# Kernel tuning notes

Measured on AMD Instinct MI355X. Metric: run time of the kernel, lower is better.

## Reference

```python
import jax, jax.numpy as jnp
import numpy as np

B, T, C, H = 2, 2048, 1024, 16
N = C // H
MISS_ROWS = 128


def _rwkv7_scan(q, w_log, k, v, a, b):
    # all [B,T,H,N] float32 (bf16-rounded). RWKV7 delta-rule recurrence:
    #   S_t = S_{t-1} * diag(exp(w_t)) + (S_{t-1} a_t) b_t^T + v_t k_t^T
    #   o_t = S_t q_t   (state S has shape [B,H,Nv,Nk]; decay along k-dim)
    Bq, Tq, Hq, Nq = q.shape

    def step(S, inp):
        q_t, w_t, k_t, v_t, a_t, b_t = inp
        ew = jnp.exp(w_t)  # decay in (0,1) since w_log = -exp(...) < 0
        sa = jnp.einsum('bhvi,bhi->bhv', S, a_t)
        S = S * ew[:, :, None, :] + sa[..., None] * b_t[:, :, None, :] + v_t[..., None] * k_t[:, :, None, :]
        o = jnp.einsum('bhvj,bhj->bhv', S, q_t)
        return S, o

    xs = tuple(jnp.moveaxis(u, 1, 0) for u in (q, w_log, k, v, a, b))
    S0 = jnp.zeros((Bq, Hq, Nq, Nq), jnp.float32)
    _, o = jax.lax.scan(step, S0, xs)
    return jnp.moveaxis(o, 0, 1)  # [B,T,H,N]


def setup_inputs() -> dict:
    key = jax.random.key(0)
    ks = jax.random.split(key, 16)
    f32 = jnp.float32
    return {
        'residual': jax.random.normal(ks[0], (B, T, C), f32),
        'x': jax.random.normal(ks[1], (B, T, C), f32),
        'x0': jax.random.normal(ks[2], (B, T, C), f32),
        'dx0': jax.random.normal(ks[3], (B, T, C), f32),
        'Wq': jax.random.normal(ks[4], (C, C), f32) * 0.02,
        'Wk': jax.random.normal(ks[5], (C, C), f32) * 0.02,
        'Wv': jax.random.normal(ks[6], (C, C), f32) * 0.02,
        'Wproj': jax.random.normal(ks[7], (C, C), f32) * 0.02,
        'x_q': jax.random.uniform(ks[8], (1, 1, C), f32),
        'x_k': jax.random.uniform(ks[9], (1, 1, C), f32),
        'x_v': jax.random.uniform(ks[10], (1, 1, C), f32),
        'v0': 0.7 + 0.1 * jax.random.normal(ks[11], (1, 1, C), f32),
        'w0': -3.0 + 0.5 * jax.random.normal(ks[12], (1, 1, C), f32),
        'a0': 0.1 * jax.random.normal(ks[13], (1, 1, C), f32),
        'miss': jax.random.normal(ks[14], (MISS_ROWS, 4 * C), f32) * 0.02,
        'r_k': 0.1 * jax.random.normal(ks[15], (H, N), f32),
    }


def reference(residual, x, x0, dx0, Wq, Wk, Wv, Wproj, x_q, x_k, x_v, v0, w0, a0, miss, r_k):
    Bx, Tx, Cx = x.shape
    Hh, Nn = r_k.shape
    # token shift: dx_prev = x_{t-1} - x_t (zero-padded at t=0)
    dx_prev = jnp.concatenate([jnp.zeros_like(x[:, :1]), x[:, :-1]], axis=1) - x
    q = (x + dx_prev * x_q) @ Wq.T
    k = (x + dx_prev * x_k) @ Wk.T
    v = (x + dx_prev * x_v) @ Wv.T
    deltas = x[:, :, :miss.shape[0]] @ miss  # [B,T,4C]
    w_delta, v_delta, a_delta, g = jnp.split(deltas, 4, axis=-1)
    log_neglog_w = -jax.nn.softplus(-(w0 + w_delta)) - 0.5
    log_w = -jnp.exp(log_neglog_w)  # log decay, always < 0
    v_first = (x0 + dx0 * x_v) @ Wv.T
    v = v + (v_first - v) * jax.nn.sigmoid(v0 + v_delta)
    g = 1.0 + g
    a = jax.nn.sigmoid(a0 + a_delta)
    kh = k.reshape(Bx, Tx, Hh, Nn)
    kk = kh / jnp.maximum(jnp.linalg.norm(kh, axis=-1, keepdims=True), 1e-12)
    kk = kk.reshape(Bx, Tx, Cx)
    k = k * a
    z = -kk
    b = kk * a
    bf = lambda u: u.astype(jnp.bfloat16).astype(jnp.float32).reshape(Bx, Tx, Hh, Nn)
    qh, wh, kh2, vh, zh, bh = (bf(u) for u in (q, log_w, k, v, z, b))
    y = _rwkv7_scan(qh, wh, kh2, vh, zh, bh) * (float(Nn) ** -0.5)  # [B,T,H,N]
    xnorm = jnp.linalg.norm(x.reshape(Bx, Tx, Hh, Nn), axis=-1, keepdims=True)
    vnorm = jnp.linalg.norm(vh, axis=-1, keepdims=True)
    u = (1.0 - xnorm / (vnorm + 1e-12)) * jax.nn.sigmoid(r_k)
    y = (y + vh * u).reshape(Bx, Tx, Cx)
    y = y * g
    return residual + y @ Wproj.T
```

## Files before the change

kernel.cpp:

```cpp
#include <hip/hip_runtime.h>
#include <stdint.h>
#include <stddef.h>

#define B_ 2
#define T_ 2048
#define C_ 1024
#define H_ 16
#define N_ 64
#define M_ (B_*T_)
#define L_ 128
#define NC_ (T_/L_)

typedef unsigned short ushort_t;
typedef __attribute__((ext_vector_type(8))) __bf16 bf16x8;
typedef __attribute__((ext_vector_type(4))) float  f32x4;

__device__ __forceinline__ ushort_t f2bf(float x){
  uint32_t u = __float_as_uint(x);
  u += 0x7fffu + ((u >> 16) & 1u);
  return (ushort_t)(u >> 16);
}
__device__ __forceinline__ float bf2f(uint32_t hu){
  return __uint_as_float(hu << 16);
}
__device__ __forceinline__ float quad_sum(float v){
  float a = __int_as_float(__builtin_amdgcn_mov_dpp(__float_as_int(v), 0xB1, 0xF, 0xF, true));
  v += a;
  float b = __int_as_float(__builtin_amdgcn_mov_dpp(__float_as_int(v), 0x4E, 0xF, 0xF, true));
  return v + b;
}

__device__ __forceinline__ ushort4 mixq4(float4 a, float4 p, float4 c){
  ushort4 o;
  o.x = f2bf(fmaf(p.x - a.x, c.x, a.x));
  o.y = f2bf(fmaf(p.y - a.y, c.y, a.y));
  o.z = f2bf(fmaf(p.z - a.z, c.z, a.z));
  o.w = f2bf(fmaf(p.w - a.w, c.w, a.w));
  return o;
}
__global__ __launch_bounds__(256) void prep_all(
    const float* __restrict__ x, const float* __restrict__ x0,
    const float* __restrict__ dx0,
    const float* __restrict__ xq, const float* __restrict__ xk,
    const float* __restrict__ xv,
    const float* __restrict__ Wq, const float* __restrict__ Wk,
    const float* __restrict__ Wv, const float* __restrict__ Wp,
    const float* __restrict__ miss,
    ushort_t* __restrict__ Aq, ushort_t* __restrict__ Ak,
    ushort_t* __restrict__ Av, ushort_t* __restrict__ Axf,
    ushort_t* __restrict__ Xb,
    ushort_t* __restrict__ Wb, ushort_t* __restrict__ Wpb,
    ushort_t* __restrict__ missT)
{
  __shared__ ushort_t tile[128][66];
  const int blk = blockIdx.x;
  const int tid = threadIdx.x;
  if (blk < 4096){
    const int idx = blk*256 + tid;
    const int col4 = idx & 255;
    const int i = idx >> 8;
    const int t = i & (T_-1);
    float4 a = ((const float4*)x)[idx];
    float4 p = {0.f,0.f,0.f,0.f};
    if (t > 0) p = ((const float4*)x)[idx - 256];
    float4 cq = ((const float4*)xq)[col4];
    float4 ck = ((const float4*)xk)[col4];
    float4 cv = ((const float4*)xv)[col4];
    ((ushort4*)Aq)[idx] = mixq4(a, p, cq);
    ((ushort4*)Ak)[idx] = mixq4(a, p, ck);
    ((ushort4*)Av)[idx] = mixq4(a, p, cv);
    float4 z = ((const float4*)x0)[idx];
    float4 d = ((const float4*)dx0)[idx];
    ushort4 of;
    of.x = f2bf(fmaf(d.x, cv.x, z.x));
    of.y = f2bf(fmaf(d.y, cv.y, z.y));
    of.z = f2bf(fmaf(d.z, cv.z, z.z));
    of.w = f2bf(fmaf(d.w, cv.w, z.w));
    ((ushort4*)Axf)[idx] = of;
    ushort4 ob = {f2bf(a.x), f2bf(a.y), f2bf(a.z), f2bf(a.w)};
    ((ushort4*)Xb)[idx] = ob;
  } else if (blk < 4096 + 5*1024){
    const int y = (blk - 4096) >> 10;
    const float* src = (y==0)?Wq:(y==1)?Wk:(y<4)?Wv:Wp;
    ushort_t* dst = (y<4) ? Wb + (size_t)y*C_*C_ : Wpb;
    const int idx = ((blk - 4096) & 1023)*256 + tid;
    float4 v = ((const float4*)src)[idx];
    ushort4 o = {f2bf(v.x), f2bf(v.y), f2bf(v.z), f2bf(v.w)};
    ((ushort4*)dst)[idx] = o;
  } else {
    const int j0 = (blk - 4096 - 5*1024)*64;
#pragma unroll
    for (int rep=0; rep<8; rep++){
      int k = rep*16 + (tid>>4);
      int jj = (tid&15)*4;
      float4 v = *(const float4*)&miss[(size_t)k*4096 + j0 + jj];
      tile[k][jj+0]=f2bf(v.x); tile[k][jj+1]=f2bf(v.y);
      tile[k][jj+2]=f2bf(v.z); tile[k][jj+3]=f2bf(v.w);
    }
    __syncthreads();
#pragma unroll
    for (int rep=0; rep<8; rep++){
      int j = tid>>2;
      int kk = (tid&3)*32 + rep*4;
      ushort4 o = {tile[kk+0][j], tile[kk+1][j], tile[kk+2][j], tile[kk+3][j]};
      *(ushort4*)&missT[(size_t)(j0+j)*128 + kk] = o;
    }
  }
}

__global__ __launch_bounds__(256, 2) void mfma_gemm(
    const ushort_t* __restrict__ Ab, int lda, int64_t Asz,
    const ushort_t* __restrict__ Bbp, int ldb, int64_t Bsz,
    void* __restrict__ Cb, int ldc, int64_t Csz, int c_bf16,
    const float* __restrict__ resid, int K)
{
  const ushort_t* A  = Ab  + (size_t)blockIdx.z * Asz;
  const ushort_t* Bm = Bbp + (size_t)blockIdx.z * Bsz;
  const int i0 = blockIdx.y * 128;
  const int j0 = blockIdx.x * 128;
  const int tid = threadIdx.x;
  const int lane = tid & 63;
  const int w = tid >> 6;
  const int wm = w & 1, wn = w >> 1;

  __shared__ ushort_t As[128*32];
  __shared__ ushort_t Bs[128*32];

  f32x4 acc[4][4];
#pragma unroll
  for (int i=0;i<4;i++)
#pragma unroll
    for (int j=0;j<4;j++) acc[i][j] = (f32x4){0.f,0.f,0.f,0.f};

  const int lr = lane >> 2;
  const int ls = lane & 3;
  const ushort_t* ga = A  + (size_t)(i0 + w*32 + lr)*lda + ls*8;
  const ushort_t* gb = Bm + (size_t)(j0 + w*32 + lr)*ldb + ls*8;
  const int lm = lane & 15, lq = lane >> 4;

  for (int k0 = 0; k0 < K; k0 += 32){
    __syncthreads();
#pragma unroll
    for (int p=0;p<2;p++){
      __builtin_amdgcn_global_load_lds(
        (const __attribute__((address_space(1))) void*)(ga + (size_t)p*16*lda + k0),
        (__attribute__((address_space(3))) void*)&As[(w*32 + p*16)*32], 16, 0, 0);
      __builtin_amdgcn_global_load_lds(
        (const __attribute__((address_space(1))) void*)(gb + (size_t)p*16*ldb + k0),
        (__attribute__((address_space(3))) void*)&Bs[(w*32 + p*16)*32], 16, 0, 0);
    }
    __syncthreads();
    bf16x8 af[4], bfr[4];
#pragma unroll
    for (int i=0;i<4;i++)
      af[i] = *(const bf16x8*)&As[(wm*64 + i*16 + lm)*32 + lq*8];
#pragma unroll
    for (int j=0;j<4;j++)
      bfr[j] = *(const bf16x8*)&Bs[(wn*64 + j*16 + lm)*32 + lq*8];
#pragma unroll
    for (int i=0;i<4;i++)
#pragma unroll
      for (int j=0;j<4;j++)
        acc[i][j] = __builtin_amdgcn_mfma_f32_16x16x32_bf16(af[i], bfr[j], acc[i][j], 0, 0, 0);
  }

  if (!c_bf16){
    float* C = (float*)Cb + (size_t)blockIdx.z * Csz;
#pragma unroll
    for (int i=0;i<4;i++)
#pragma unroll
      for (int j=0;j<4;j++)
#pragma unroll
        for (int r=0;r<4;r++){
          const int row = i0 + wm*64 + i*16 + lq*4 + r;
          const int col = j0 + wn*64 + j*16 + lm;
          float v = acc[i][j][r];
          if (resid) v += resid[(size_t)row*ldc + col];
          C[(size_t)row*ldc + col] = v;
        }
  } else {
    ushort_t* C = (ushort_t*)Cb + (size_t)blockIdx.z * Csz;
#pragma unroll
    for (int i=0;i<4;i++)
#pragma unroll
      for (int j=0;j<4;j++)
#pragma unroll
        for (int r=0;r<4;r++){
          const int row = i0 + wm*64 + i*16 + lq*4 + r;
          const int col = j0 + wn*64 + j*16 + lm;
          C[(size_t)row*ldc + col] = f2bf(acc[i][j][r]);
        }
  }
}

__global__ __launch_bounds__(256, 2) void qkvm_gemm(
    const ushort_t* __restrict__ Ab4, const ushort_t* __restrict__ Wb,
    const ushort_t* __restrict__ Xb,  const ushort_t* __restrict__ missT,
    float* __restrict__ qkvf, ushort_t* __restrict__ delb)
{
  const int bid = blockIdx.x;
  const bool isQKV = bid < 1024;
  const ushort_t* A; const ushort_t* Bm;
  int i0, j0, ldb, K, z = 0;
  if (isQKV){
    z = bid >> 8;
    const int g = bid & 255;
    j0 = (g & 7) * 128;
    i0 = (g >> 3) * 128;
    A  = Ab4 + (size_t)z*M_*C_;
    Bm = Wb  + (size_t)z*C_*C_;
    ldb = C_; K = C_;
  } else {
    const int g = bid - 1024;
    j0 = (g & 31) * 128;
    i0 = (g >> 5) * 128;
    A = Xb; Bm = missT;
    ldb = 128; K = 128;
  }
  const int lda = C_;
  const int tid = threadIdx.x;
  const int lane = tid & 63;
  const int w = tid >> 6;
  const int wm = w & 1, wn = w >> 1;

  __shared__ ushort_t As[128*32];
  __shared__ ushort_t Bs[128*32];

  f32x4 acc[4][4];
#pragma unroll
  for (int i=0;i<4;i++)
#pragma unroll
    for (int j=0;j<4;j++) acc[i][j] = (f32x4){0.f,0.f,0.f,0.f};

  const int lr = lane >> 2;
  const int ls = lane & 3;
  const ushort_t* ga = A  + (size_t)(i0 + w*32 + lr)*lda + ls*8;
  const ushort_t* gb = Bm + (size_t)(j0 + w*32 + lr)*ldb + ls*8;
  const int lm = lane & 15, lq = lane >> 4;

  for (int k0 = 0; k0 < K; k0 += 32){
    __syncthreads();
#pragma unroll
    for (int p=0;p<2;p++){
      __builtin_amdgcn_global_load_lds(
        (const __attribute__((address_space(1))) void*)(ga + (size_t)p*16*lda + k0),
        (__attribute__((address_space(3))) void*)&As[(w*32 + p*16)*32], 16, 0, 0);
      __builtin_amdgcn_global_load_lds(
        (const __attribute__((address_space(1))) void*)(gb + (size_t)p*16*ldb + k0),
        (__attribute__((address_space(3))) void*)&Bs[(w*32 + p*16)*32], 16, 0, 0);
    }
    __syncthreads();
    bf16x8 af[4], bfr[4];
#pragma unroll
    for (int i=0;i<4;i++)
      af[i] = *(const bf16x8*)&As[(wm*64 + i*16 + lm)*32 + lq*8];
#pragma unroll
    for (int j=0;j<4;j++)
      bfr[j] = *(const bf16x8*)&Bs[(wn*64 + j*16 + lm)*32 + lq*8];
#pragma unroll
    for (int i=0;i<4;i++)
#pragma unroll
      for (int j=0;j<4;j++)
        acc[i][j] = __builtin_amdgcn_mfma_f32_16x16x32_bf16(af[i], bfr[j], acc[i][j], 0, 0, 0);
  }

  if (isQKV){
    float* C = qkvf + (size_t)z*M_*C_;
#pragma unroll
    for (int i=0;i<4;i++)
#pragma unroll
      for (int j=0;j<4;j++)
#pragma unroll
        for (int r=0;r<4;r++){
          const int row = i0 + wm*64 + i*16 + lq*4 + r;
          const int col = j0 + wn*64 + j*16 + lm;
          C[(size_t)row*C_ + col] = acc[i][j][r];
        }
  } else {
#pragma unroll
    for (int i=0;i<4;i++)
#pragma unroll
      for (int j=0;j<4;j++)
#pragma unroll
        for (int r=0;r<4;r++){
          const int row = i0 + wm*64 + i*16 + lq*4 + r;
          const int col = j0 + wn*64 + j*16 + lm;
          delb[(size_t)row*(4*C_) + col] = f2bf(acc[i][j][r]);
        }
  }
}


__global__ __launch_bounds__(512, 4) void chunk_mdp_kernel(
    const float* __restrict__ qm, const float* __restrict__ km,
    const float* __restrict__ vm, const float* __restrict__ vfm,
    const float* __restrict__ x, const ushort_t* __restrict__ delb,
    const float* __restrict__ w0, const float* __restrict__ v0,
    const float* __restrict__ a0,
    float* __restrict__ phi, float* __restrict__ cc, float* __restrict__ md,
    ushort_t* __restrict__ vb, float* __restrict__ ratio)
{
  const int tid  = threadIdx.x;
  const int role = tid >> 8;
  const int row  = (tid >> 2) & 63;
  const int qr   = tid & 3;

  __shared__ float ewS[8][N_], zS[8][N_], bS[8][N_], kS[8][N_], qS[8][N_], vS[8][N_];

  const int g  = blockIdx.x;
  const int cx = g & (NC_-1), bh = g >> 4;
  const int b = bh >> 4, h = bh & 15;
  const int t0 = b*T_ + cx*L_;

  const int ls = tid >> 6;
  const int ld = tid & 63;
  const int cdim = h*64 + ld;
  const float w0c = w0[cdim], v0c = v0[cdim], a0c = a0[cdim];

  float pq, pk, pv, pvf, px;
  ushort_t dwd, dvd, dad;
  float Few, Fz, Fb, Fk, Fq, Fv, Fratio;
  ushort_t Fvr;

#define LOAD_RAW(T_IDX) { \
    size_t ic = (size_t)(t0 + (T_IDX))*C_ + cdim; \
    pq = qm[ic]; pk = km[ic]; pv = vm[ic]; pvf = vfm[ic]; px = x[ic]; \
    size_t d0 = (size_t)(t0 + (T_IDX))*4*C_ + cdim; \
    dwd = delb[d0]; dvd = delb[d0+C_]; dad = delb[d0+2*C_]; }

#define FUSE_RAW() { \
    float wd = bf2f(dwd), vd = bf2f(dvd), ad = bf2f(dad); \
    float z1 = -(w0c + wd); \
    float sp = fmaxf(z1, 0.f) + log1pf(expf(-fabsf(z1))); \
    float logw = -expf(-sp - 0.5f); \
    float sv = 1.f/(1.f+expf(-(v0c + vd))); \
    float vvm = pv + (pvf - pv)*sv; \
    float av = 1.f/(1.f+expf(-(a0c + ad))); \
    Fvr = f2bf(vvm); \
    float vrf = bf2f(Fvr); \
    float ksq = pk*pk, xsq = px*px, vsq = vrf*vrf; \
    _Pragma("unroll") \
    for (int off=32; off>0; off>>=1){ \
      ksq += __shfl_xor(ksq, off, 64); \
      xsq += __shfl_xor(xsq, off, 64); \
      vsq += __shfl_xor(vsq, off, 64); \
    } \
    float kn = sqrtf(ksq); \
    float kkn = pk / fmaxf(kn, 1e-12f); \
    Few = __expf(bf2f(f2bf(logw))); \
    Fz = bf2f(f2bf(-kkn)); \
    Fb = bf2f(f2bf(kkn*av)); \
    Fk = bf2f(f2bf(pk*av)); \
    Fq = bf2f(f2bf(pq)); \
    Fv = vrf; \
    Fratio = 1.f - sqrtf(xsq)/(sqrtf(vsq)+1e-12f); }

  LOAD_RAW(ls);
  FUSE_RAW();

  float R[16];
  if (role == 0){
#pragma unroll
    for (int i=0;i<16;i++) R[i] = (qr*16+i == row) ? 1.f : 0.f;
  } else {
#pragma unroll
    for (int i=0;i<16;i++) R[i] = 0.f;
  }

  for (int tg = 0; tg < L_; tg += 8){
    __syncthreads();
    ewS[ls][ld] = Few;
    zS[ls][ld]  = Fz;
    bS[ls][ld]  = Fb;
    kS[ls][ld]  = Fk;
    qS[ls][ld]  = Fq;
    vS[ls][ld]  = Fv;
    {
      const int tok = t0 + tg + ls;
      vb[(size_t)tok*C_ + cdim] = Fvr;
      if (ld == 0)
        ratio[(size_t)tok*H_ + h] = Fratio;
    }
    if (tg + 8 < L_) LOAD_RAW(tg+8+ls);
    __syncthreads();
#pragma unroll 1
    for (int ss=0; ss<8; ss++){
      const float* zr = &zS[ss][qr*16];
      float s_ = 0.f;
#pragma unroll
      for (int i4=0;i4<4;i4++){
        float4 z4 = *(const float4*)&zr[i4*4];
        s_ = fmaf(R[i4*4+0], z4.x, s_);
        s_ = fmaf(R[i4*4+1], z4.y, s_);
        s_ = fmaf(R[i4*4+2], z4.z, s_);
        s_ = fmaf(R[i4*4+3], z4.w, s_);
      }
      s_ = quad_sum(s_);
      const float* er = &ewS[ss][qr*16];
      const float* br = &bS[ss][qr*16];
      const float* qrp = &qS[ss][qr*16];
      float o = 0.f;
      if (role == 0){
#pragma unroll
        for (int i4=0;i4<4;i4++){
          float4 e4 = *(const float4*)&er[i4*4];
          float4 b4 = *(const float4*)&br[i4*4];
          float4 q4 = *(const float4*)&qrp[i4*4];
          float t;
          t = fmaf(R[i4*4+0], e4.x, s_*b4.x); R[i4*4+0]=t; o = fmaf(t, q4.x, o);
          t = fmaf(R[i4*4+1], e4.y, s_*b4.y); R[i4*4+1]=t; o = fmaf(t, q4.y, o);
          t = fmaf(R[i4*4+2], e4.z, s_*b4.z); R[i4*4+2]=t; o = fmaf(t, q4.z, o);
          t = fmaf(R[i4*4+3], e4.w, s_*b4.w); R[i4*4+3]=t; o = fmaf(t, q4.w, o);
        }
      } else {
        const float* kr = &kS[ss][qr*16];
        const float vr = vS[ss][row];
#pragma unroll
        for (int i4=0;i4<4;i4++){
          float4 e4 = *(const float4*)&er[i4*4];
          float4 b4 = *(const float4*)&br[i4*4];
          float4 q4 = *(const float4*)&qrp[i4*4];
          float4 k4 = *(const float4*)&kr[i4*4];
          float t;
          t = fmaf(R[i4*4+0], e4.x, fmaf(s_, b4.x, vr*k4.x)); R[i4*4+0]=t; o = fmaf(t, q4.x, o);
          t = fmaf(R[i4*4+1], e4.y, fmaf(s_, b4.y, vr*k4.y)); R[i4*4+1]=t; o = fmaf(t, q4.y, o);
          t = fmaf(R[i4*4+2], e4.z, fmaf(s_, b4.z, vr*k4.z)); R[i4*4+2]=t; o = fmaf(t, q4.z, o);
          t = fmaf(R[i4*4+3], e4.w, fmaf(s_, b4.w, vr*k4.w)); R[i4*4+3]=t; o = fmaf(t, q4.w, o);
        }
      }
      o = quad_sum(o);
      if (qr == 0)
        md[((size_t)g*L_ + tg+ss)*128 + role*64 + row] = o;
    }
    if (tg + 8 < L_) FUSE_RAW();
  }
  float* dst = (role == 0) ? phi : cc;
  const size_t base = (size_t)g*4096 + (size_t)row*64 + qr*16;
#pragma unroll
  for (int i4=0;i4<4;i4++)
    *(float4*)&dst[base + i4*4] = (float4){R[i4*4+0],R[i4*4+1],R[i4*4+2],R[i4*4+3]};
#undef LOAD_RAW
#undef FUSE_RAW
}

__global__ __launch_bounds__(256) void chunk_state_kernel(
    const float* __restrict__ phi, const float* __restrict__ cc,
    float* __restrict__ sstart)
{
  const int mq = blockIdx.x;
  const int bh = blockIdx.y;
  const int tid = threadIdx.x;
  const int rb = tid >> 4;
  const int cq = tid & 15;
  const int row = mq*16 + rb;
  __shared__ float Sld[16][65];
  __shared__ float Fld[64][68];
  float acc[4] = {0.f, 0.f, 0.f, 0.f};
  *(float4*)&Sld[rb][cq*4] = (float4){0.f,0.f,0.f,0.f};
  const float* pc = phi + (size_t)bh*NC_*4096;
  const float* cb = cc  + (size_t)bh*NC_*4096;
  float4 pf[4], pcc;
#pragma unroll
  for (int p=0;p<4;p++) pf[p] = *(const float4*)&pc[(size_t)p*1024 + tid*4];
  pcc = *(const float4*)&cb[(size_t)row*64 + cq*4];

  for (int c=0;c<NC_;c++){
    __syncthreads();
#pragma unroll
    for (int p=0;p<4;p++){
      int f = p*1024 + tid*4;
      *(float4*)&Fld[f>>6][f&63] = pf[p];
    }
    float na[4] = {pcc.x, pcc.y, pcc.z, pcc.w};
    *(float4*)&sstart[(size_t)(bh*NC_+c)*4096 + (size_t)row*64 + cq*4] =
        (float4){acc[0],acc[1],acc[2],acc[3]};
    if (c+1 < NC_){
#pragma unroll
      for (int p=0;p<4;p++) pf[p] = *(const float4*)&pc[(size_t)(c+1)*4096 + p*1024 + tid*4];
      pcc = *(const float4*)&cb[(size_t)(c+1)*4096 + (size_t)row*64 + cq*4];
    }
    __syncthreads();
#pragma unroll 1
    for (int k0=0;k0<64;k0+=4){
      const float4 sr = *(const float4*)&Sld[rb][k0];
      const float4 f0 = *(const float4*)&Fld[k0+0][cq*4];
      const float4 f1 = *(const float4*)&Fld[k0+1][cq*4];
      const float4 f2 = *(const float4*)&Fld[k0+2][cq*4];
      const float4 f3 = *(const float4*)&Fld[k0+3][cq*4];
      na[0] = fmaf(sr.x, f0.x, na[0]); na[0] = fmaf(sr.y, f1.x, na[0]);
      na[0] = fmaf(sr.z, f2.x, na[0]); na[0] = fmaf(sr.w, f3.x, na[0]);
      na[1] = fmaf(sr.x, f0.y, na[1]); na[1] = fmaf(sr.y, f1.y, na[1]);
      na[1] = fmaf(sr.z, f2.y, na[1]); na[1] = fmaf(sr.w, f3.y, na[1]);
      na[2] = fmaf(sr.x, f0.z, na[2]); na[2] = fmaf(sr.y, f1.z, na[2]);
      na[2] = fmaf(sr.z, f2.z, na[2]); na[2] = fmaf(sr.w, f3.z, na[2]);
      na[3] = fmaf(sr.x, f0.w, na[3]); na[3] = fmaf(sr.y, f1.w, na[3]);
      na[3] = fmaf(sr.z, f2.w, na[3]); na[3] = fmaf(sr.w, f3.w, na[3]);
    }
    __syncthreads();
    *(float4*)&Sld[rb][cq*4] = (float4){na[0],na[1],na[2],na[3]};
#pragma unroll
    for (int i=0;i<4;i++) acc[i] = na[i];
  }
}

__global__ __launch_bounds__(256) void chunk_emit_kernel(
    const ushort_t* __restrict__ vb, const ushort_t* __restrict__ delb,
    const float* __restrict__ ratio, const float* __restrict__ rk,
    const float* __restrict__ sstart, const float* __restrict__ md,
    ushort_t* __restrict__ y)
{
  const int blk = blockIdx.x;
  const int c  = blk & (NC_-1);
  const int bh = blk >> 4;
  const int b = bh >> 4, h = bh & 15;
  const int tid = threadIdx.x;
  const int v = tid & 63;
  const int tg = tid >> 6;

  float4 sr[16];
  const float4* sp = (const float4*)(sstart + (size_t)blk*4096 + (size_t)v*64);
#pragma unroll
  for (int f=0;f<16;f++) sr[f] = sp[f];
  const float sigrk = 1.f/(1.f+__expf(-rk[h*64+v]));

#pragma unroll 1
  for (int ss=0; ss<32; ss++){
    const int t = tg*32 + ss;
    const int token = b*T_ + c*L_ + t;
    const float* mrow = md + ((size_t)blk*L_ + t)*128;
    float o0=0.f,o1=0.f,o2=0.f,o3=0.f;
#pragma unroll
    for (int f=0;f<16;f+=4){
      float4 m0 = ((const float4*)mrow)[f+0];
      float4 m1 = ((const float4*)mrow)[f+1];
      float4 m2 = ((const float4*)mrow)[f+2];
      float4 m3 = ((const float4*)mrow)[f+3];
      o0 = fmaf(sr[f+0].x,m0.x, fmaf(sr[f+0].y,m0.y, fmaf(sr[f+0].z,m0.z, fmaf(sr[f+0].w,m0.w, o0))));
      o1 = fmaf(sr[f+1].x,m1.x, fmaf(sr[f+1].y,m1.y, fmaf(sr[f+1].z,m1.z, fmaf(sr[f+1].w,m1.w, o1))));
      o2 = fmaf(sr[f+2].x,m2.x, fmaf(sr[f+2].y,m2.y, fmaf(sr[f+2].z,m2.z, fmaf(sr[f+2].w,m2.w, o2))));
      o3 = fmaf(sr[f+3].x,m3.x, fmaf(sr[f+3].y,m3.y, fmaf(sr[f+3].z,m3.z, fmaf(sr[f+3].w,m3.w, o3))));
    }
    float o = ((o0+o1)+(o2+o3)) + mrow[64 + v];
    const float vt = bf2f(vb[(size_t)token*C_ + h*64 + v]);
    const float uv = ratio[(size_t)token*H_ + h];
    const float gv = 1.f + bf2f(delb[(size_t)token*4*C_ + 3*C_ + h*64 + v]);
    y[(size_t)token*C_ + h*64 + v] = f2bf((o*0.125f + vt*uv*sigrk)*gv);
  }
}

extern "C" void kernel_launch(void* const* d_in, const int* in_sizes, int n_in,
                              void* d_out, int out_size, void* d_ws, size_t ws_size,
                              hipStream_t stream)
{
  const float* residual = (const float*)d_in[0];
  const float* x    = (const float*)d_in[1];
  const float* x0   = (const float*)d_in[2];
  const float* dx0  = (const float*)d_in[3];
  const float* Wq   = (const float*)d_in[4];
  const float* Wk   = (const float*)d_in[5];
  const float* Wv   = (const float*)d_in[6];
  const float* Wpr  = (const float*)d_in[7];
  const float* x_q  = (const float*)d_in[8];
  const float* x_k  = (const float*)d_in[9];
  const float* x_v  = (const float*)d_in[10];
  const float* v0   = (const float*)d_in[11];
  const float* w0   = (const float*)d_in[12];
  const float* a0   = (const float*)d_in[13];
  const float* miss = (const float*)d_in[14];
  const float* rk   = (const float*)d_in[15];
  float* out = (float*)d_out;

  char* ws = (char*)d_ws;
  const size_t MB = (size_t)1 << 20;
  float*    q_m    = (float*)(ws + 0*MB);
  float*    k_m    = (float*)(ws + 16*MB);
  float*    v_m    = (float*)(ws + 32*MB);
  float*    vf_m   = (float*)(ws + 48*MB);
  ushort_t* delb   = (ushort_t*)(ws + 64*MB);
  ushort_t* Ab     = (ushort_t*)(ws + 96*MB);
  ushort_t* Xb     = (ushort_t*)(ws + 128*MB);
  ushort_t* Wb     = (ushort_t*)(ws + 136*MB);
  ushort_t* Wpb    = (ushort_t*)(ws + 160*MB);
  ushort_t* missT  = (ushort_t*)(ws + 162*MB);
  float*    ratio  = (float*)(ws + 163*MB);
  float*    mdbuf  = (float*)(ws + 96*MB);
  float*    phi    = (float*)(ws + 128*MB);
  float*    cc     = (float*)(ws + 136*MB);
  float*    sstart = (float*)(ws + 144*MB);
  ushort_t* vb     = (ushort_t*)(ws + 152*MB);
  ushort_t* yb     = (ushort_t*)(ws + 48*MB);

  ushort_t* Aq  = Ab + 0*(size_t)M_*C_;
  ushort_t* Ak  = Ab + 1*(size_t)M_*C_;
  ushort_t* Av  = Ab + 2*(size_t)M_*C_;
  ushort_t* Axf = Ab + 3*(size_t)M_*C_;

  dim3 blk(256);
  prep_all<<<4096 + 5*1024 + 64, blk, 0, stream>>>(
      x, x0, dx0, x_q, x_k, x_v, Wq, Wk, Wv, Wpr, miss,
      Aq, Ak, Av, Axf, Xb, Wb, Wpb, missT);
  qkvm_gemm<<<2048, blk, 0, stream>>>(Ab, Wb, Xb, missT, q_m, delb);
  chunk_mdp_kernel<<<B_*H_*NC_, dim3(512), 0, stream>>>(
      q_m, k_m, v_m, vf_m, x, delb, w0, v0, a0, phi, cc, mdbuf, vb, ratio);
  chunk_state_kernel<<<dim3(4, B_*H_), blk, 0, stream>>>(phi, cc, sstart);
  chunk_emit_kernel<<<B_*H_*NC_, blk, 0, stream>>>(vb, delb, ratio, rk, sstart, mdbuf, yb);
  mfma_gemm<<<dim3(C_/128, M_/128, 1), blk, 0, stream>>>(
      yb, C_, 0, Wpb, C_, 0, out, C_, 0, 0, residual, C_);
}
```

Baseline: 478.7 us.

## Warp-specialize chunk kernel with producer warps and double-buffered shared inputs

Splits the chunk recurrence kernel into 512 consumer threads that run the state recurrence and 256 producer threads that load and fuse the per-token decay/key/value inputs into double-buffered shared memory. Previously every thread did both the loading/transcendental fusion and the recurrence serially within each group of eight tokens. The change is meant to overlap global loads and the exp/log work with the serial FMA recurrence. The cost is a larger block (768 threads), doubled shared buffers, and a launch bound of 8 that may force register pressure on the 16-register state.

```diff
diff --git a/kernel.cpp b/kernel.cpp
--- a/kernel.cpp
+++ b/kernel.cpp
@@ -291,7 +291,7 @@
 }
 
 
-__global__ __launch_bounds__(512, 4) void chunk_mdp_kernel(
+__global__ __launch_bounds__(768, 8) void chunk_mdp_kernel(
     const float* __restrict__ qm, const float* __restrict__ km,
     const float* __restrict__ vm, const float* __restrict__ vfm,
     const float* __restrict__ x, const ushort_t* __restrict__ delb,
@@ -300,147 +300,184 @@
     float* __restrict__ phi, float* __restrict__ cc, float* __restrict__ md,
     ushort_t* __restrict__ vb, float* __restrict__ ratio)
 {
-  const int tid  = threadIdx.x;
-  const int role = tid >> 8;
-  const int row  = (tid >> 2) & 63;
-  const int qr   = tid & 3;
-
-  __shared__ float ewS[8][N_], zS[8][N_], bS[8][N_], kS[8][N_], qS[8][N_], vS[8][N_];
+  const int tid = threadIdx.x;
+  __shared__ float ewS[2][8][N_], zS[2][8][N_], bS[2][8][N_],
+                   kS[2][8][N_], qS[2][8][N_], vS[2][8][N_];
 
   const int g  = blockIdx.x;
   const int cx = g & (NC_-1), bh = g >> 4;
   const int b = bh >> 4, h = bh & 15;
   const int t0 = b*T_ + cx*L_;
-
-  const int ls = tid >> 6;
-  const int ld = tid & 63;
-  const int cdim = h*64 + ld;
-  const float w0c = w0[cdim], v0c = v0[cdim], a0c = a0[cdim];
-
-  float pq, pk, pv, pvf, px;
-  ushort_t dwd, dvd, dad;
-  float Few, Fz, Fb, Fk, Fq, Fv, Fratio;
-  ushort_t Fvr;
-
-#define LOAD_RAW(T_IDX) { \
-    size_t ic = (size_t)(t0 + (T_IDX))*C_ + cdim; \
-    pq = qm[ic]; pk = km[ic]; pv = vm[ic]; pvf = vfm[ic]; px = x[ic]; \
-    size_t d0 = (size_t)(t0 + (T_IDX))*4*C_ + cdim; \
-    dwd = delb[d0]; dvd = delb[d0+C_]; dad = delb[d0+2*C_]; }
-
-#define FUSE_RAW() { \
-    float wd = bf2f(dwd), vd = bf2f(dvd), ad = bf2f(dad); \
-    float z1 = -(w0c + wd); \
-    float sp = fmaxf(z1, 0.f) + log1pf(expf(-fabsf(z1))); \
-    float logw = -expf(-sp - 0.5f); \
-    float sv = 1.f/(1.f+expf(-(v0c + vd))); \
-    float vvm = pv + (pvf - pv)*sv; \
-    float av = 1.f/(1.f+expf(-(a0c + ad))); \
-    Fvr = f2bf(vvm); \
-    float vrf = bf2f(Fvr); \
-    float ksq = pk*pk, xsq = px*px, vsq = vrf*vrf; \
+  const int NG = L_/8;
+
+  if (tid < 512){
+    const int role = tid >> 8;
+    const int row  = (tid >> 2) & 63;
+    const int qr   = tid & 3;
+    float R[16];
+    if (role == 0){
+#pragma unroll
+      for (int i=0;i<16;i++) R[i] = (qr*16+i == row) ? 1.f : 0.f;
+    } else {
+#pragma unroll
+      for (int i=0;i<16;i++) R[i] = 0.f;
+    }
+
+#define COMPUTE(BUF, GRP) { \
+    _Pragma("unroll 1") \
+    for (int ss=0; ss<8; ss++){ \
+      const float* zr = &zS[BUF][ss][qr*16]; \
+      float s_ = 0.f; \
+      _Pragma("unroll") \
+      for (int i4=0;i4<4;i4++){ \
+        float4 z4 = *(const float4*)&zr[i4*4]; \
+        s_ = fmaf(R[i4*4+0], z4.x, s_); \
+        s_ = fmaf(R[i4*4+1], z4.y, s_); \
+        s_ = fmaf(R[i4*4+2], z4.z, s_); \
+        s_ = fmaf(R[i4*4+3], z4.w, s_); \
+      } \
+      s_ = quad_sum(s_); \
+      const float* er = &ewS[BUF][ss][qr*16]; \
+      const float* br = &bS[BUF][ss][qr*16]; \
+      const float* qrp = &qS[BUF][ss][qr*16]; \
+      float o = 0.f; \
+      if (role == 0){ \
+        _Pragma("unroll") \
+        for (int i4=0;i4<4;i4++){ \
+          float4 e4 = *(const float4*)&er[i4*4]; \
+          float4 b4 = *(const float4*)&br[i4*4]; \
+          float4 q4 = *(const float4*)&qrp[i4*4]; \
+          float t; \
+          t = fmaf(R[i4*4+0], e4.x, s_*b4.x); R[i4*4+0]=t; o = fmaf(t, q4.x, o); \
+          t = fmaf(R[i4*4+1], e4.y, s_*b4.y); R[i4*4+1]=t; o = fmaf(t, q4.y, o); \
+          t = fmaf(R[i4*4+2], e4.z, s_*b4.z); R[i4*4+2]=t; o = fmaf(t, q4.z, o); \
+          t = fmaf(R[i4*4+3], e4.w, s_*b4.w); R[i4*4+3]=t; o = fmaf(t, q4.w, o); \
+        } \
+      } else { \
+        const float* kr = &kS[BUF][ss][qr*16]; \
+        const float vr = vS[BUF][ss][row]; \
+        _Pragma("unroll") \
+        for (int i4=0;i4<4;i4++){ \
+          float4 e4 = *(const float4*)&er[i4*4]; \
+          float4 b4 = *(const float4*)&br[i4*4]; \
+          float4 q4 = *(const float4*)&qrp[i4*4]; \
+          float4 k4 = *(const float4*)&kr[i4*4]; \
+          float t; \
+          t = fmaf(R[i4*4+0], e4.x, fmaf(s_, b4.x, vr*k4.x)); R[i4*4+0]=t; o = fmaf(t, q4.x, o); \
+          t = fmaf(R[i4*4+1], e4.y, fmaf(s_, b4.y, vr*k4.y)); R[i4*4+1]=t; o = fmaf(t, q4.y, o); \
+          t = fmaf(R[i4*4+2], e4.z, fmaf(s_, b4.z, vr*k4.z)); R[i4*4+2]=t; o = fmaf(t, q4.z, o); \
+          t = fmaf(R[i4*4+3], e4.w, fmaf(s_, b4.w, vr*k4.w)); R[i4*4+3]=t; o = fmaf(t, q4.w, o); \
+        } \
+      } \
+      o = quad_sum(o); \
+      if (qr == 0) \
+        md[((size_t)g*L_ + (GRP)*8+ss)*128 + role*64 + row] = o; \
+    } }
+
+    __syncthreads();
+#pragma unroll 1
+    for (int pair = 0; pair < NG/2; ++pair){
+      COMPUTE(0, pair*2);
+      __syncthreads();
+      COMPUTE(1, pair*2+1);
+      __syncthreads();
+    }
+#undef COMPUTE
+    float* dst = (role == 0) ? phi : cc;
+    const size_t base = (size_t)g*4096 + (size_t)row*64 + qr*16;
+#pragma unroll
+    for (int i4=0;i4<4;i4++)
+      *(float4*)&dst[base + i4*4] = (float4){R[i4*4+0],R[i4*4+1],R[i4*4+2],R[i4*4+3]};
+  } else {
+    const int ptid = tid - 512;
+    const int pw = ptid >> 6;
+    const int pl = ptid & 63;
+    const int cdim = h*64 + pl;
+    const float w0c = w0[cdim], v0c = v0[cdim], a0c = a0[cdim];
+
+    float pq[2], pk[2], pv[2], pvf[2], px[2];
+    ushort_t dwd[2], dvd[2], dad[2];
+    float Few[2], Fz[2], Fb[2], Fk[2], Fq[2], Fv[2], Fratio[2];
+    ushort_t Fvr[2];
+
+#define LOAD_RAW(GRP) { \
     _Pragma("unroll") \
-    for (int off=32; off>0; off>>=1){ \
-      ksq += __shfl_xor(ksq, off, 64); \
-      xsq += __shfl_xor(xsq, off, 64); \
-      vsq += __shfl_xor(vsq, off, 64); \
-    } \
-    float kn = sqrtf(ksq); \
-    float kkn = pk / fmaxf(kn, 1e-12f); \
-    Few = __expf(bf2f(f2bf(logw))); \
-    Fz = bf2f(f2bf(-kkn)); \
-    Fb = bf2f(f2bf(kkn*av)); \
-    Fk = bf2f(f2bf(pk*av)); \
-    Fq = bf2f(f2bf(pq)); \
-    Fv = vrf; \
-    Fratio = 1.f - sqrtf(xsq)/(sqrtf(vsq)+1e-12f); }
-
-  LOAD_RAW(ls);
-  FUSE_RAW();
-
-  float R[16];
-  if (role == 0){
-#pragma unroll
-    for (int i=0;i<16;i++) R[i] = (qr*16+i == row) ? 1.f : 0.f;
-  } else {
-#pragma unroll
-    for (int i=0;i<16;i++) R[i] = 0.f;
-  }
-
-  for (int tg = 0; tg < L_; tg += 8){
-    __syncthreads();
-    ewS[ls][ld] = Few;
-    zS[ls][ld]  = Fz;
-    bS[ls][ld]  = Fb;
-    kS[ls][ld]  = Fk;
-    qS[ls][ld]  = Fq;
-    vS[ls][ld]  = Fv;
-    {
-      const int tok = t0 + tg + ls;
-      vb[(size_t)tok*C_ + cdim] = Fvr;
-      if (ld == 0)
-        ratio[(size_t)tok*H_ + h] = Fratio;
-    }
-    if (tg + 8 < L_) LOAD_RAW(tg+8+ls);
+    for (int i=0;i<2;i++){ \
+      int tok = t0 + (GRP)*8 + pw + i*4; \
+      size_t ic = (size_t)tok*C_ + cdim; \
+      pq[i] = qm[ic]; pk[i] = km[ic]; pv[i] = vm[ic]; pvf[i] = vfm[ic]; px[i] = x[ic]; \
+      size_t d0 = (size_t)tok*4*C_ + cdim; \
+      dwd[i] = delb[d0]; dvd[i] = delb[d0+C_]; dad[i] = delb[d0+2*C_]; \
+    } }
+
+#define FUSE_ALL() { \
+    _Pragma("unroll") \
+    for (int i=0;i<2;i++){ \
+      float wd = bf2f(dwd[i]), vd = bf2f(dvd[i]), ad = bf2f(dad[i]); \
+      float z1 = -(w0c + wd); \
+      float sp = fmaxf(z1, 0.f) + log1pf(expf(-fabsf(z1))); \
+      float logw = -expf(-sp - 0.5f); \
+      float sv = 1.f/(1.f+expf(-(v0c + vd))); \
+      float vvm = pv[i] + (pvf[i] - pv[i])*sv; \
+      float av = 1.f/(1.f+expf(-(a0c + ad))); \
+      Fvr[i] = f2bf(vvm); \
+      float vrf = bf2f(Fvr[i]); \
+      float ksq = pk[i]*pk[i], xsq = px[i]*px[i], vsq = vrf*vrf; \
+      _Pragma("unroll") \
+      for (int off=32; off>0; off>>=1){ \
+        ksq += __shfl_xor(ksq, off, 64); \
+        xsq += __shfl_xor(xsq, off, 64); \
+        vsq += __shfl_xor(vsq, off, 64); \
+      } \
+      float kn = sqrtf(ksq); \
+      float kkn = pk[i] / fmaxf(kn, 1e-12f); \
+      Few[i] = __expf(bf2f(f2bf(logw))); \
+      Fz[i]  = bf2f(f2bf(-kkn)); \
+      Fb[i]  = bf2f(f2bf(kkn*av)); \
+      Fk[i]  = bf2f(f2bf(pk[i]*av)); \
+      Fq[i]  = bf2f(f2bf(pq[i])); \
+      Fv[i]  = vrf; \
+      Fratio[i] = 1.f - sqrtf(xsq)/(sqrtf(vsq)+1e-12f); \
+    } }
+
+#define WRITE_F(BUF, GRP) { \
+    _Pragma("unroll") \
+    for (int i=0;i<2;i++){ \
+      int st = pw + i*4; \
+      ewS[BUF][st][pl] = Few[i]; \
+      zS[BUF][st][pl]  = Fz[i]; \
+      bS[BUF][st][pl]  = Fb[i]; \
+      kS[BUF][st][pl]  = Fk[i]; \
+      qS[BUF][st][pl]  = Fq[i]; \
+      vS[BUF][st][pl]  = Fv[i]; \
+      int tok = t0 + (GRP)*8 + st; \
+      vb[(size_t)tok*C_ + cdim] = Fvr[i]; \
+      if (pl == 0) ratio[(size_t)tok*H_ + h] = Fratio[i]; \
+    } }
+
+    LOAD_RAW(0);
+    FUSE_ALL();
+    WRITE_F(0, 0);
+    LOAD_RAW(1);
     __syncthreads();
 #pragma unroll 1
-    for (int ss=0; ss<8; ss++){
-      const float* zr = &zS[ss][qr*16];
-      float s_ = 0.f;
-#pragma unroll
-      for (int i4=0;i4<4;i4++){
-        float4 z4 = *(const float4*)&zr[i4*4];
-        s_ = fmaf(R[i4*4+0], z4.x, s_);
-        s_ = fmaf(R[i4*4+1], z4.y, s_);
-        s_ = fmaf(R[i4*4+2], z4.z, s_);
-        s_ = fmaf(R[i4*4+3], z4.w, s_);
+    for (int pair = 0; pair < NG/2; ++pair){
+      const int gB = pair*2 + 1;
+      FUSE_ALL();
+      WRITE_F(1, gB);
+      if (gB + 1 < NG) LOAD_RAW(gB + 1);
+      __syncthreads();
+      if (gB + 1 < NG){
+        FUSE_ALL();
+        WRITE_F(0, gB + 1);
+        if (gB + 2 < NG) LOAD_RAW(gB + 2);
       }
-      s_ = quad_sum(s_);
-      const float* er = &ewS[ss][qr*16];
-      const float* br = &bS[ss][qr*16];
-      const float* qrp = &qS[ss][qr*16];
-      float o = 0.f;
-      if (role == 0){
-#pragma unroll
-        for (int i4=0;i4<4;i4++){
-          float4 e4 = *(const float4*)&er[i4*4];
-          float4 b4 = *(const float4*)&br[i4*4];
-          float4 q4 = *(const float4*)&qrp[i4*4];
-          float t;
-          t = fmaf(R[i4*4+0], e4.x, s_*b4.x); R[i4*4+0]=t; o = fmaf(t, q4.x, o);
-          t = fmaf(R[i4*4+1], e4.y, s_*b4.y); R[i4*4+1]=t; o = fmaf(t, q4.y, o);
-          t = fmaf(R[i4*4+2], e4.z, s_*b4.z); R[i4*4+2]=t; o = fmaf(t, q4.z, o);
-          t = fmaf(R[i4*4+3], e4.w, s_*b4.w); R[i4*4+3]=t; o = fmaf(t, q4.w, o);
-        }
-      } else {
-        const float* kr = &kS[ss][qr*16];
-        const float vr = vS[ss][row];
-#pragma unroll
-        for (int i4=0;i4<4;i4++){
-          float4 e4 = *(const float4*)&er[i4*4];
-          float4 b4 = *(const float4*)&br[i4*4];
-          float4 q4 = *(const float4*)&qrp[i4*4];
-          float4 k4 = *(const float4*)&kr[i4*4];
-          float t;
-          t = fmaf(R[i4*4+0], e4.x, fmaf(s_, b4.x, vr*k4.x)); R[i4*4+0]=t; o = fmaf(t, q4.x, o);
-          t = fmaf(R[i4*4+1], e4.y, fmaf(s_, b4.y, vr*k4.y)); R[i4*4+1]=t; o = fmaf(t, q4.y, o);
-          t = fmaf(R[i4*4+2], e4.z, fmaf(s_, b4.z, vr*k4.z)); R[i4*4+2]=t; o = fmaf(t, q4.z, o);
-          t = fmaf(R[i4*4+3], e4.w, fmaf(s_, b4.w, vr*k4.w)); R[i4*4+3]=t; o = fmaf(t, q4.w, o);
-        }
-      }
-      o = quad_sum(o);
-      if (qr == 0)
-        md[((size_t)g*L_ + tg+ss)*128 + role*64 + row] = o;
-    }
-    if (tg + 8 < L_) FUSE_RAW();
-  }
-  float* dst = (role == 0) ? phi : cc;
-  const size_t base = (size_t)g*4096 + (size_t)row*64 + qr*16;
-#pragma unroll
-  for (int i4=0;i4<4;i4++)
-    *(float4*)&dst[base + i4*4] = (float4){R[i4*4+0],R[i4*4+1],R[i4*4+2],R[i4*4+3]};
+      __syncthreads();
+    }
 #undef LOAD_RAW
-#undef FUSE_RAW
+#undef FUSE_ALL
+#undef WRITE_F
+  }
 }
 
 __global__ __launch_bounds__(256) void chunk_state_kernel(
@@ -600,7 +637,7 @@
       x, x0, dx0, x_q, x_k, x_v, Wq, Wk, Wv, Wpr, miss,
       Aq, Ak, Av, Axf, Xb, Wb, Wpb, missT);
   qkvm_gemm<<<2048, blk, 0, stream>>>(Ab, Wb, Xb, missT, q_m, delb);
-  chunk_mdp_kernel<<<B_*H_*NC_, dim3(512), 0, stream>>>(
+  chunk_mdp_kernel<<<B_*H_*NC_, dim3(768), 0, stream>>>(
       q_m, k_m, v_m, vf_m, x, delb, w0, v0, a0, phi, cc, mdbuf, vb, ratio);
   chunk_state_kernel<<<dim3(4, B_*H_), blk, 0, stream>>>(phi, cc, sstart);
   chunk_emit_kernel<<<B_*H_*NC_, blk, 0, stream>>>(vb, delb, ratio, rk, sstart, mdbuf, yb);
```

Result: faster. 461.4 us (-3.6%).
